# Optimization experiments

Hardware: AMD Instinct MI355X
Metric: run time of the kernel (lower is better)

Reference implementation:

```python
import jax, jax.numpy as jnp
import numpy as np

N = 100000
IN_C = 128
HID_C = 128
OUT_C = 128
E = 3200000


def setup_inputs() -> dict:
    key = jax.random.key(0)
    ks = jax.random.split(key, 8)
    x = jax.random.normal(ks[0], (N, IN_C), dtype=jnp.float32)
    edge_index = jax.random.randint(ks[1], (2, E), 0, N, dtype=jnp.int64)
    edge_weight = jnp.ones((E,), dtype=jnp.float32)
    s = 1.0 / np.sqrt(HID_C)
    W_conv = jax.random.uniform(ks[2], (HID_C, IN_C), jnp.float32, -s, s)
    b_conv = jnp.zeros((HID_C,), dtype=jnp.float32)
    W_fc = jax.random.uniform(ks[3], (HID_C, HID_C), jnp.float32, -s, s)
    b_fc = jax.random.uniform(ks[4], (HID_C,), jnp.float32, -s, s)
    W_fc2 = jax.random.uniform(ks[5], (OUT_C, HID_C), jnp.float32, -s, s)
    b_fc2 = jax.random.uniform(ks[6], (OUT_C,), jnp.float32, -s, s)
    return {"x": x, "edge_index": edge_index, "edge_weight": edge_weight,
            "W_conv": W_conv, "b_conv": b_conv, "W_fc": W_fc, "b_fc": b_fc,
            "W_fc2": W_fc2, "b_fc2": b_fc2}


def _gcn_conv(x, edge_index, edge_weight, W_conv, b_conv):
    n = x.shape[0]
    # add self-loops with weight 1 (PyG GCNConv default)
    loop = jnp.arange(n, dtype=edge_index.dtype)
    src = jnp.concatenate([edge_index[0], loop])
    dst = jnp.concatenate([edge_index[1], loop])
    ew = jnp.concatenate([edge_weight, jnp.ones((n,), dtype=edge_weight.dtype)])
    # symmetric normalization: deg^-1/2[src] * w * deg^-1/2[dst]
    deg = jax.ops.segment_sum(ew, dst, num_segments=n)
    dinv = jnp.where(deg > 0, jax.lax.rsqrt(jnp.where(deg > 0, deg, 1.0)), 0.0)
    norm = dinv[src] * ew * dinv[dst]  # [E+N]
    h = x @ W_conv.T                   # [N, hid], bias-free linear first
    msg = h[src] * norm[:, None]       # gather + scale
    agg = jax.ops.segment_sum(msg, dst, num_segments=n)  # scatter-add
    return agg + b_conv


def reference(x, edge_index, edge_weight, W_conv, b_conv, W_fc, b_fc, W_fc2, b_fc2):
    h = _gcn_conv(x, edge_index, edge_weight, W_conv, b_conv)
    h = jax.nn.relu(h)
    h = jax.nn.relu(h @ W_fc.T + b_fc)
    return h @ W_fc2.T + b_fc2
```

## Files before the change

kernel.cpp:

```cpp
#include <hip/hip_runtime.h>

typedef short bf16x8 __attribute__((ext_vector_type(8)));
typedef short bf16x4 __attribute__((ext_vector_type(4)));
typedef float f32x4 __attribute__((ext_vector_type(4)));
typedef float f32x2 __attribute__((ext_vector_type(2)));

#define PS 32
#define PMAX 4096
#define CAPP 1312
#define NB 256

__device__ __forceinline__ unsigned short f2bf(float f) {
    unsigned int u = __float_as_uint(f);
    u = (u + 0x7FFFu + ((u >> 16) & 1u)) >> 16;
    return (unsigned short)u;
}

__global__ __launch_bounds__(1024) void scat_k(const int* __restrict__ ei,
                                               const float* __restrict__ ew,
                                               int* __restrict__ partCnt,
                                               int2* __restrict__ regions,
                                               const float* __restrict__ Wc,
                                               const float* __restrict__ Wf,
                                               const float* __restrict__ W2,
                                               unsigned short* __restrict__ wcb,
                                               unsigned short* __restrict__ wfb,
                                               unsigned short* __restrict__ w2b,
                                               int E, int P, int EPB) {
    __shared__ int cntl[PMAX];
    __shared__ int basel[PMAX];
    const int b = blockIdx.x, tid = threadIdx.x;

    if (b < 12) {
        int t = (b << 10) | tid;
        int a = t >> 12, idx = t & 4095;
        const float4* s4 = (const float4*)(a == 0 ? Wc : (a == 1 ? Wf : W2));
        unsigned short* dw = (a == 0 ? wcb : (a == 1 ? wfb : w2b));
        float4 v = s4[idx];
        ushort4 o;
        o.x = f2bf(v.x); o.y = f2bf(v.y); o.z = f2bf(v.z); o.w = f2bf(v.w);
        *(ushort4*)(dw + idx * 4) = o;
    }

    for (int i = tid; i < P; i += 1024) cntl[i] = 0;
    __syncthreads();
    const int s = b * EPB, e = min(E, s + EPB);
    for (int i = s + tid; i < e; i += 1024)
        atomicAdd(&cntl[ei[E + i] >> 5], 1);
    __syncthreads();
    for (int p = tid; p < P; p += 1024) {
        int c = cntl[p];
        basel[p] = p * CAPP + (c ? atomicAdd(&partCnt[p], c) : 0);
        cntl[p] = 0;
    }
    __syncthreads();
    for (int i = s + tid; i < e; i += 1024) {
        int src = ei[i];
        int dst = ei[E + i];
        float w = ew[i];
        int p = dst >> 5, dl = dst & 31;
        int lidx = atomicAdd(&cntl[p], 1);
        int pos = basel[p] + lidx;
        if (pos < (p + 1) * CAPP)
            regions[pos] = make_int2(src | (dl << 24), __float_as_int(w));
    }
}

__global__ __launch_bounds__(256) void dgemm1_k(const float* __restrict__ x,
                                                const unsigned short* __restrict__ Wcb,
                                                const int* __restrict__ partCnt,
                                                const int2* __restrict__ regions,
                                                float* __restrict__ dinv,
                                                int* __restrict__ nodeOff,
                                                unsigned short* __restrict__ h,
                                                int M, int P) {
    __shared__ __align__(16) unsigned short Wl[128 * 136];
    __shared__ float degl[256];
    __shared__ int cl[256];
    const int tid = threadIdx.x;
    degl[tid] = 0.f; cl[tid] = 0;

#pragma unroll
    for (int i = 0; i < 8; ++i) {
        int c = i * 256 + tid;
        int r = c >> 4, col = (c & 15) * 8;
        *(bf16x8*)&Wl[r * 136 + col] = *(const bf16x8*)(Wcb + c * 8);
    }
    __syncthreads();

#pragma unroll
    for (int q = 0; q < 8; ++q) {
        int p = blockIdx.x * 8 + q;
        if (p < P) {
            const int cnt = min(partCnt[p], CAPP);
            const int2* reg = regions + (size_t)p * CAPP;
            for (int i = tid; i < cnt; i += 256) {
                int2 r = reg[i];
                int dl = q * 32 + ((r.x >> 24) & 31);
                atomicAdd(&cl[dl], 1);
                atomicAdd(&degl[dl], __int_as_float(r.y));
            }
        }
    }
    __syncthreads();
    {
        int l32 = tid & 31;
        int cn = cl[tid];
        int v = cn;
#pragma unroll
        for (int off = 1; off < 32; off <<= 1) {
            int u = __shfl_up(v, off, 32);
            if (l32 >= off) v += u;
        }
        int node = blockIdx.x * 256 + tid;
        float d = rsqrtf(1.0f + degl[tid]);
        if (node < M) { nodeOff[node] = v - cn; dinv[node] = d; }
        degl[tid] = d;
    }
    __syncthreads();

    const int wave = tid >> 6, lane = tid & 63;
    const int m = lane & 15, quad = lane >> 4;

#pragma unroll
    for (int t = 0; t < 4; ++t) {
        const int tileBase = blockIdx.x * 256 + t * 64;
        if (tileBase >= M) break;
        const int rowBase = tileBase + wave * 16;
        int arow = rowBase + m;
        int arowc = arow < M ? arow : (M - 1);

        bf16x8 afrag[4];
        const float* pa = x + (size_t)arowc * 128 + quad * 8;
#pragma unroll
        for (int kc = 0; kc < 4; ++kc) {
            float4 v0 = *(const float4*)(pa + kc * 32);
            float4 v1 = *(const float4*)(pa + kc * 32 + 4);
            bf16x8 f;
            f[0] = (short)f2bf(v0.x); f[1] = (short)f2bf(v0.y);
            f[2] = (short)f2bf(v0.z); f[3] = (short)f2bf(v0.w);
            f[4] = (short)f2bf(v1.x); f[5] = (short)f2bf(v1.y);
            f[6] = (short)f2bf(v1.z); f[7] = (short)f2bf(v1.w);
            afrag[kc] = f;
        }

        float dv[4];
#pragma unroll
        for (int r = 0; r < 4; ++r)
            dv[r] = degl[t * 64 + wave * 16 + quad * 4 + r];

#pragma unroll
        for (int nt = 0; nt < 8; ++nt) {
            f32x4 acc = {0.f, 0.f, 0.f, 0.f};
            const unsigned short* wb = &Wl[(nt * 16 + m) * 136 + quad * 8];
#pragma unroll
            for (int kc = 0; kc < 4; ++kc) {
                bf16x8 bfrag = *(const bf16x8*)(wb + kc * 32);
                acc = __builtin_amdgcn_mfma_f32_16x16x32_bf16(afrag[kc], bfrag, acc, 0, 0, 0);
            }
            const int col = nt * 16 + m;
#pragma unroll
            for (int r = 0; r < 4; ++r) {
                int row = rowBase + quad * 4 + r;
                if (row < M)
                    h[((size_t)(col >> 6) * M + row) * 64 + (col & 63)] = f2bf(acc[r] * dv[r]);
            }
        }
    }
}

__global__ __launch_bounds__(256) void aggF_k(const int* __restrict__ partCnt,
                                              const int* __restrict__ nodeOff,
                                              const int2* __restrict__ regions,
                                              const unsigned short* __restrict__ h,
                                              const float* __restrict__ dinv,
                                              const float* __restrict__ bconv,
                                              unsigned short* __restrict__ h2, int N) {
    __shared__ __align__(16) int2 stag[CAPP];
    __shared__ int cstart[PS + 1];
    __shared__ int wcur[PS];
    const int p = blockIdx.x, tid = threadIdx.x;
    const int cnt = min(partCnt[p], CAPP);
    const int2* reg = regions + (size_t)p * CAPP;

    if (tid < PS) {
        int node = p * PS + tid;
        int o = (node < N) ? nodeOff[node] : cnt;
        cstart[tid] = o;
        wcur[tid] = o;
    } else if (tid == PS) {
        cstart[PS] = cnt;
    }
    __syncthreads();
    for (int i = tid; i < cnt; i += 256) {
        int2 r = reg[i];
        int pos = atomicAdd(&wcur[(r.x >> 24) & 31], 1);
        stag[pos] = make_int2((r.x & 0xFFFFFF) << 7, r.y);
    }
    __syncthreads();

    const int wave = tid >> 6, lane = tid & 63;
    const int g = lane >> 4;
    const int c4 = (lane & 15) * 4;
    const int c4b = c4 * 2;

#define ACC2(q, w) {                                                        \
        unsigned ux = (unsigned)(q).x, uy = (unsigned)(q).y;                \
        f32x2 ww; ww[0] = (w); ww[1] = (w);                                 \
        f32x2 v01, v23;                                                     \
        v01[0] = __uint_as_float(ux << 16);                                 \
        v01[1] = __uint_as_float(ux & 0xFFFF0000u);                         \
        v23[0] = __uint_as_float(uy << 16);                                 \
        v23[1] = __uint_as_float(uy & 0xFFFF0000u);                         \
        a01 = v01 * ww + a01; a23 = v23 * ww + a23; }

#pragma unroll
    for (int hh = 0; hh < 2; ++hh) {
        const char* hb = (const char*)h + ((size_t)hh * (size_t)N << 7);
        for (int nl = wave; nl < PS; nl += 4) {
            int n = p * PS + nl;
            if (n >= N) continue;
            const int s = cstart[nl], e = cstart[nl + 1];
            f32x2 a01 = {0.f, 0.f}, a23 = {0.f, 0.f};
            int j = s;
            const int e32 = s + ((e - s) & ~31);
            for (; j < e32; j += 32) {
                int2 r0 = stag[j + g];
                int2 r1 = stag[j + 4 + g];
                int2 r2 = stag[j + 8 + g];
                int2 r3 = stag[j + 12 + g];
                int2 r4 = stag[j + 16 + g];
                int2 r5 = stag[j + 20 + g];
                int2 r6 = stag[j + 24 + g];
                int2 r7 = stag[j + 28 + g];
                int2 q0 = *(const int2*)(hb + ((unsigned)r0.x + c4b));
                int2 q1 = *(const int2*)(hb + ((unsigned)r1.x + c4b));
                int2 q2 = *(const int2*)(hb + ((unsigned)r2.x + c4b));
                int2 q3 = *(const int2*)(hb + ((unsigned)r3.x + c4b));
                int2 q4 = *(const int2*)(hb + ((unsigned)r4.x + c4b));
                int2 q5 = *(const int2*)(hb + ((unsigned)r5.x + c4b));
                int2 q6 = *(const int2*)(hb + ((unsigned)r6.x + c4b));
                int2 q7 = *(const int2*)(hb + ((unsigned)r7.x + c4b));
                ACC2(q0, __int_as_float(r0.y));
                ACC2(q1, __int_as_float(r1.y));
                ACC2(q2, __int_as_float(r2.y));
                ACC2(q3, __int_as_float(r3.y));
                ACC2(q4, __int_as_float(r4.y));
                ACC2(q5, __int_as_float(r5.y));
                ACC2(q6, __int_as_float(r6.y));
                ACC2(q7, __int_as_float(r7.y));
            }
            const int e16 = s + ((e - s) & ~15);
            for (; j < e16; j += 16) {
                int2 r0 = stag[j + g];
                int2 r1 = stag[j + 4 + g];
                int2 r2 = stag[j + 8 + g];
                int2 r3 = stag[j + 12 + g];
                int2 q0 = *(const int2*)(hb + ((unsigned)r0.x + c4b));
                int2 q1 = *(const int2*)(hb + ((unsigned)r1.x + c4b));
                int2 q2 = *(const int2*)(hb + ((unsigned)r2.x + c4b));
                int2 q3 = *(const int2*)(hb + ((unsigned)r3.x + c4b));
                ACC2(q0, __int_as_float(r0.y));
                ACC2(q1, __int_as_float(r1.y));
                ACC2(q2, __int_as_float(r2.y));
                ACC2(q3, __int_as_float(r3.y));
            }
            for (; j < e; j += 8) {
                int j0 = j + g, j1 = j + 4 + g;
                int2 r0 = stag[j0 < e ? j0 : s];
                int2 r1 = stag[j1 < e ? j1 : s];
                float w0 = (j0 < e) ? __int_as_float(r0.y) : 0.f;
                float w1 = (j1 < e) ? __int_as_float(r1.y) : 0.f;
                int2 q0 = *(const int2*)(hb + ((unsigned)r0.x + c4b));
                int2 q1 = *(const int2*)(hb + ((unsigned)r1.x + c4b));
                ACC2(q0, w0);
                ACC2(q1, w1);
            }
            float acc[4] = {a01[0], a01[1], a23[0], a23[1]};
#pragma unroll
            for (int k = 0; k < 4; ++k) {
                float v = acc[k];
                v += __shfl_xor(v, 16, 64);
                v += __shfl_xor(v, 32, 64);
                acc[k] = v;
            }
            if (g == 0) {
                float di = dinv[n];
                int2 qs = *(const int2*)(hb + (((size_t)(unsigned)n << 7) + c4b));
                float4 b = *(const float4*)(bconv + hh * 64 + c4);
                unsigned ux = (unsigned)qs.x, uy = (unsigned)qs.y;
                bf16x4 o;
                o[0] = (short)f2bf(fmaxf(di * (acc[0] + __uint_as_float(ux << 16)) + b.x, 0.f));
                o[1] = (short)f2bf(fmaxf(di * (acc[1] + __uint_as_float(ux & 0xFFFF0000u)) + b.y, 0.f));
                o[2] = (short)f2bf(fmaxf(di * (acc[2] + __uint_as_float(uy << 16)) + b.z, 0.f));
                o[3] = (short)f2bf(fmaxf(di * (acc[3] + __uint_as_float(uy & 0xFFFF0000u)) + b.w, 0.f));
                *(bf16x4*)(h2 + (size_t)n * 128 + hh * 64 + c4) = o;
            }
        }
    }
#undef ACC2
}

__global__ __launch_bounds__(256) void gemm23_k(const unsigned short* __restrict__ h2,
                                                const unsigned short* __restrict__ Wfb,
                                                const float* __restrict__ bfc,
                                                const unsigned short* __restrict__ W2b,
                                                const float* __restrict__ b2,
                                                float* __restrict__ out, int M) {
    __shared__ __align__(16) unsigned short Wl[128 * 136];
    __shared__ __align__(16) unsigned short Tl[64 * 136];
    const int tid = threadIdx.x;

#pragma unroll
    for (int i = 0; i < 8; ++i) {
        int c = i * 256 + tid;
        int r = c >> 4, col = (c & 15) * 8;
        *(bf16x8*)&Wl[r * 136 + col] = *(const bf16x8*)(Wfb + c * 8);
    }
    __syncthreads();

    const int wave = tid >> 6, lane = tid & 63;
    const int m = lane & 15, quad = lane >> 4;
    const int rowBase = blockIdx.x * 64 + wave * 16;
    int arow = rowBase + m;
    int arowc = arow < M ? arow : (M - 1);

    bf16x8 afrag[4];
    {
        const unsigned short* pa = h2 + (size_t)arowc * 128 + quad * 8;
#pragma unroll
        for (int kc = 0; kc < 4; ++kc)
            afrag[kc] = *(const bf16x8*)(pa + kc * 32);
    }

#pragma unroll
    for (int nt = 0; nt < 8; ++nt) {
        f32x4 acc = {0.f, 0.f, 0.f, 0.f};
        const unsigned short* wb = &Wl[(nt * 16 + m) * 136 + quad * 8];
#pragma unroll
        for (int kc = 0; kc < 4; ++kc) {
            bf16x8 bfrag = *(const bf16x8*)(wb + kc * 32);
            acc = __builtin_amdgcn_mfma_f32_16x16x32_bf16(afrag[kc], bfrag, acc, 0, 0, 0);
        }
        const int col = nt * 16 + m;
        float bv = bfc[col];
#pragma unroll
        for (int r = 0; r < 4; ++r) {
            int rowl = wave * 16 + quad * 4 + r;
            Tl[rowl * 136 + col] = f2bf(fmaxf(acc[r] + bv, 0.f));
        }
    }
    __syncthreads();

#pragma unroll
    for (int i = 0; i < 8; ++i) {
        int c = i * 256 + tid;
        int r = c >> 4, col = (c & 15) * 8;
        *(bf16x8*)&Wl[r * 136 + col] = *(const bf16x8*)(W2b + c * 8);
    }
    __syncthreads();

    bf16x8 afrag2[4];
    {
        const unsigned short* pa = &Tl[(wave * 16 + m) * 136 + quad * 8];
#pragma unroll
        for (int kc = 0; kc < 4; ++kc)
            afrag2[kc] = *(const bf16x8*)(pa + kc * 32);
    }
#pragma unroll
    for (int nt = 0; nt < 8; ++nt) {
        f32x4 acc = {0.f, 0.f, 0.f, 0.f};
        const unsigned short* wb = &Wl[(nt * 16 + m) * 136 + quad * 8];
#pragma unroll
        for (int kc = 0; kc < 4; ++kc) {
            bf16x8 bfrag = *(const bf16x8*)(wb + kc * 32);
            acc = __builtin_amdgcn_mfma_f32_16x16x32_bf16(afrag2[kc], bfrag, acc, 0, 0, 0);
        }
        const int col = nt * 16 + m;
        float bv = b2[col];
#pragma unroll
        for (int r = 0; r < 4; ++r) {
            int row = rowBase + quad * 4 + r;
            if (row < M)
                out[(size_t)row * 128 + col] = acc[r] + bv;
        }
    }
}

extern "C" void kernel_launch(void* const* d_in, const int* in_sizes, int n_in,
                              void* d_out, int out_size, void* d_ws, size_t ws_size,
                              hipStream_t stream) {
    const float* x  = (const float*)d_in[0];
    const int* ei   = (const int*)d_in[1];
    const float* ew = (const float*)d_in[2];
    const float* Wc = (const float*)d_in[3];
    const float* bc = (const float*)d_in[4];
    const float* Wf = (const float*)d_in[5];
    const float* bf = (const float*)d_in[6];
    const float* W2 = (const float*)d_in[7];
    const float* b2 = (const float*)d_in[8];
    float* out = (float*)d_out;

    const int N = in_sizes[0] / 128;
    const int E = in_sizes[2];
    const int P = (N + PS - 1) / PS;

    auto align256 = [](size_t v) { return (v + 255) & ~(size_t)255; };
    char* ws = (char*)d_ws;
    size_t off = 0;
    float* dinv  = (float*)(ws + off); off += align256((size_t)N * 4);
    int* nodeOff = (int*)(ws + off);   off += align256((size_t)N * 4);
    int* partCnt = (int*)(ws + off);   off += align256((size_t)P * 4);
    unsigned short* wcb = (unsigned short*)(ws + off); off += align256(16384 * 2);
    unsigned short* wfb = (unsigned short*)(ws + off); off += align256(16384 * 2);
    unsigned short* w2b = (unsigned short*)(ws + off); off += align256(16384 * 2);
    unsigned short* h  = (unsigned short*)(ws + off); off += (size_t)N * 256;
    unsigned short* h2 = (unsigned short*)(ws + off);

    int2* regions = (int2*)out;

    const int EPB = (E + NB - 1) / NB;

    hipMemsetAsync(partCnt, 0, (size_t)P * 4, stream);
    scat_k<<<NB, 1024, 0, stream>>>(ei, ew, partCnt, regions, Wc, Wf, W2, wcb, wfb, w2b, E, P, EPB);
    dgemm1_k<<<(N + 255) / 256, 256, 0, stream>>>(x, wcb, partCnt, regions, dinv, nodeOff, h, N, P);
    aggF_k<<<P, 256, 0, stream>>>(partCnt, nodeOff, regions, h, dinv, bc, h2, N);
    gemm23_k<<<(N + 63) / 64, 256, 0, stream>>>(h2, wfb, bf, w2b, b2, out, N);
}
```

Before: 362.3 us.

## Compute degree with global atomics in scatter and sort edges by source within partitions

Degree accumulation moves out of the GEMM kernel, which previously re-read all partition regions, into the scatter kernel as global float atomics into a zeroed degree array. The first GEMM no longer scales by dinv; the aggregation kernel now folds the source dinv into each edge weight and applies dinv^2 to the self-loop term. Edges are counting-sorted by (destination, source-block) key so that gathers into h gain some locality. This adds 3.2M global atomics in scatter and extra dinv gathers per edge, in exchange for removing a full pass over the regions buffer.

```diff
diff --git a/kernel.cpp b/kernel.cpp
--- a/kernel.cpp
+++ b/kernel.cpp
@@ -19,6 +19,7 @@
 __global__ __launch_bounds__(1024) void scat_k(const int* __restrict__ ei,
                                                const float* __restrict__ ew,
                                                int* __restrict__ partCnt,
+                                               float* __restrict__ deg,
                                                int2* __restrict__ regions,
                                                const float* __restrict__ Wc,
                                                const float* __restrict__ Wf,
@@ -59,6 +60,7 @@
         int dst = ei[E + i];
         float w = ew[i];
         int p = dst >> 5, dl = dst & 31;
+        atomicAdd(&deg[dst], w);
         int lidx = atomicAdd(&cntl[p], 1);
         int pos = basel[p] + lidx;
         if (pos < (p + 1) * CAPP)
@@ -68,54 +70,23 @@
 
 __global__ __launch_bounds__(256) void dgemm1_k(const float* __restrict__ x,
                                                 const unsigned short* __restrict__ Wcb,
-                                                const int* __restrict__ partCnt,
-                                                const int2* __restrict__ regions,
+                                                const float* __restrict__ deg,
                                                 float* __restrict__ dinv,
-                                                int* __restrict__ nodeOff,
                                                 unsigned short* __restrict__ h,
-                                                int M, int P) {
+                                                int M) {
     __shared__ __align__(16) unsigned short Wl[128 * 136];
-    __shared__ float degl[256];
-    __shared__ int cl[256];
     const int tid = threadIdx.x;
-    degl[tid] = 0.f; cl[tid] = 0;
+
+    {
+        int node = blockIdx.x * 256 + tid;
+        if (node < M) dinv[node] = rsqrtf(1.0f + deg[node]);
+    }
 
 #pragma unroll
     for (int i = 0; i < 8; ++i) {
         int c = i * 256 + tid;
         int r = c >> 4, col = (c & 15) * 8;
         *(bf16x8*)&Wl[r * 136 + col] = *(const bf16x8*)(Wcb + c * 8);
-    }
-    __syncthreads();
-
-#pragma unroll
-    for (int q = 0; q < 8; ++q) {
-        int p = blockIdx.x * 8 + q;
-        if (p < P) {
-            const int cnt = min(partCnt[p], CAPP);
-            const int2* reg = regions + (size_t)p * CAPP;
-            for (int i = tid; i < cnt; i += 256) {
-                int2 r = reg[i];
-                int dl = q * 32 + ((r.x >> 24) & 31);
-                atomicAdd(&cl[dl], 1);
-                atomicAdd(&degl[dl], __int_as_float(r.y));
-            }
-        }
-    }
-    __syncthreads();
-    {
-        int l32 = tid & 31;
-        int cn = cl[tid];
-        int v = cn;
-#pragma unroll
-        for (int off = 1; off < 32; off <<= 1) {
-            int u = __shfl_up(v, off, 32);
-            if (l32 >= off) v += u;
-        }
-        int node = blockIdx.x * 256 + tid;
-        float d = rsqrtf(1.0f + degl[tid]);
-        if (node < M) { nodeOff[node] = v - cn; dinv[node] = d; }
-        degl[tid] = d;
     }
     __syncthreads();
 
@@ -144,11 +115,6 @@
             afrag[kc] = f;
         }
 
-        float dv[4];
-#pragma unroll
-        for (int r = 0; r < 4; ++r)
-            dv[r] = degl[t * 64 + wave * 16 + quad * 4 + r];
-
 #pragma unroll
         for (int nt = 0; nt < 8; ++nt) {
             f32x4 acc = {0.f, 0.f, 0.f, 0.f};
@@ -163,39 +129,63 @@
             for (int r = 0; r < 4; ++r) {
                 int row = rowBase + quad * 4 + r;
                 if (row < M)
-                    h[((size_t)(col >> 6) * M + row) * 64 + (col & 63)] = f2bf(acc[r] * dv[r]);
+                    h[((size_t)(col >> 6) * M + row) * 64 + (col & 63)] = f2bf(acc[r]);
             }
         }
     }
 }
 
 __global__ __launch_bounds__(256) void aggF_k(const int* __restrict__ partCnt,
-                                              const int* __restrict__ nodeOff,
                                               const int2* __restrict__ regions,
                                               const unsigned short* __restrict__ h,
                                               const float* __restrict__ dinv,
                                               const float* __restrict__ bconv,
                                               unsigned short* __restrict__ h2, int N) {
     __shared__ __align__(16) int2 stag[CAPP];
+    __shared__ int c256[256];
     __shared__ int cstart[PS + 1];
-    __shared__ int wcur[PS];
     const int p = blockIdx.x, tid = threadIdx.x;
     const int cnt = min(partCnt[p], CAPP);
     const int2* reg = regions + (size_t)p * CAPP;
 
+    c256[tid] = 0;
+    __syncthreads();
+
+    int2 rr[6]; float dvv[6]; int key[6]; bool okk[6];
+#pragma unroll
+    for (int k = 0; k < 6; ++k) {
+        int i = tid + k * 256;
+        okk[k] = (i < cnt);
+        rr[k] = okk[k] ? reg[i] : make_int2(0, 0);
+        dvv[k] = okk[k] ? dinv[rr[k].x & 0xFFFFFF] : 0.f;
+        key[k] = (((rr[k].x >> 24) & 31) << 3) | ((rr[k].x & 0xFFFFFF) >> 14);
+        if (okk[k]) atomicAdd(&c256[key[k]], 1);
+    }
+    __syncthreads();
     if (tid < PS) {
-        int node = p * PS + tid;
-        int o = (node < N) ? nodeOff[node] : cnt;
-        cstart[tid] = o;
-        wcur[tid] = o;
-    } else if (tid == PS) {
-        cstart[PS] = cnt;
-    }
-    __syncthreads();
-    for (int i = tid; i < cnt; i += 256) {
-        int2 r = reg[i];
-        int pos = atomicAdd(&wcur[(r.x >> 24) & 31], 1);
-        stag[pos] = make_int2((r.x & 0xFFFFFF) << 7, r.y);
+        int s = 0;
+#pragma unroll
+        for (int c = 0; c < 8; ++c) s += c256[tid * 8 + c];
+        int v = s;
+#pragma unroll
+        for (int off = 1; off < 32; off <<= 1) {
+            int u = __shfl_up(v, off, 32);
+            if (tid >= off) v += u;
+        }
+        cstart[tid] = v - s;
+        if (tid == PS - 1) cstart[PS] = v;
+        int run = v - s;
+#pragma unroll
+        for (int c = 0; c < 8; ++c) { int t2 = c256[tid * 8 + c]; c256[tid * 8 + c] = run; run += t2; }
+    }
+    __syncthreads();
+#pragma unroll
+    for (int k = 0; k < 6; ++k) {
+        if (okk[k]) {
+            int pos = atomicAdd(&c256[key[k]], 1);
+            stag[pos] = make_int2((rr[k].x & 0xFFFFFF) << 7,
+                                  __float_as_int(__int_as_float(rr[k].y) * dvv[k]));
+        }
     }
     __syncthreads();
 
@@ -286,14 +276,15 @@
             }
             if (g == 0) {
                 float di = dinv[n];
+                float sc = di * di;
                 int2 qs = *(const int2*)(hb + (((size_t)(unsigned)n << 7) + c4b));
                 float4 b = *(const float4*)(bconv + hh * 64 + c4);
                 unsigned ux = (unsigned)qs.x, uy = (unsigned)qs.y;
                 bf16x4 o;
-                o[0] = (short)f2bf(fmaxf(di * (acc[0] + __uint_as_float(ux << 16)) + b.x, 0.f));
-                o[1] = (short)f2bf(fmaxf(di * (acc[1] + __uint_as_float(ux & 0xFFFF0000u)) + b.y, 0.f));
-                o[2] = (short)f2bf(fmaxf(di * (acc[2] + __uint_as_float(uy << 16)) + b.z, 0.f));
-                o[3] = (short)f2bf(fmaxf(di * (acc[3] + __uint_as_float(uy & 0xFFFF0000u)) + b.w, 0.f));
+                o[0] = (short)f2bf(fmaxf(di * acc[0] + sc * __uint_as_float(ux << 16) + b.x, 0.f));
+                o[1] = (short)f2bf(fmaxf(di * acc[1] + sc * __uint_as_float(ux & 0xFFFF0000u) + b.y, 0.f));
+                o[2] = (short)f2bf(fmaxf(di * acc[2] + sc * __uint_as_float(uy << 16) + b.z, 0.f));
+                o[3] = (short)f2bf(fmaxf(di * acc[3] + sc * __uint_as_float(uy & 0xFFFF0000u) + b.w, 0.f));
                 *(bf16x4*)(h2 + (size_t)n * 128 + hh * 64 + c4) = o;
             }
         }
@@ -409,8 +400,8 @@
     char* ws = (char*)d_ws;
     size_t off = 0;
     float* dinv  = (float*)(ws + off); off += align256((size_t)N * 4);
-    int* nodeOff = (int*)(ws + off);   off += align256((size_t)N * 4);
     int* partCnt = (int*)(ws + off);   off += align256((size_t)P * 4);
+    float* deg   = (float*)(ws + off); off += align256((size_t)N * 4);
     unsigned short* wcb = (unsigned short*)(ws + off); off += align256(16384 * 2);
     unsigned short* wfb = (unsigned short*)(ws + off); off += align256(16384 * 2);
     unsigned short* w2b = (unsigned short*)(ws + off); off += align256(16384 * 2);
@@ -421,9 +412,9 @@
 
     const int EPB = (E + NB - 1) / NB;
 
-    hipMemsetAsync(partCnt, 0, (size_t)P * 4, stream);
-    scat_k<<<NB, 1024, 0, stream>>>(ei, ew, partCnt, regions, Wc, Wf, W2, wcb, wfb, w2b, E, P, EPB);
-    dgemm1_k<<<(N + 255) / 256, 256, 0, stream>>>(x, wcb, partCnt, regions, dinv, nodeOff, h, N, P);
-    aggF_k<<<P, 256, 0, stream>>>(partCnt, nodeOff, regions, h, dinv, bc, h2, N);
+    hipMemsetAsync(partCnt, 0, align256((size_t)P * 4) + (size_t)N * 4, stream);
+    scat_k<<<NB, 1024, 0, stream>>>(ei, ew, partCnt, deg, regions, Wc, Wf, W2, wcb, wfb, w2b, E, P, EPB);
+    dgemm1_k<<<(N + 255) / 256, 256, 0, stream>>>(x, wcb, deg, dinv, h, N);
+    aggF_k<<<P, 256, 0, stream>>>(partCnt, regions, h, dinv, bc, h2, N);
     gemm23_k<<<(N + 63) / 64, 256, 0, stream>>>(h2, wfb, bf, w2b, b2, out, N);
 }
```

Measured after the change: 464.0 us. 28.1% more time.
